# Performance work log

Hardware: AMD Instinct MI355X
Metric: run time of the kernel (lower is better)

Reference implementation:

```python
import jax, jax.numpy as jnp
import numpy as np

N_NODES = 50000


def setup_inputs() -> dict:
    key = jax.random.key(0)
    ks = jax.random.split(key, 6)
    E = 640000
    H = 128
    data = jax.random.normal(ks[0], (N_NODES, H), dtype=jnp.float32)
    edge = jax.random.randint(ks[1], (2, E), 0, N_NODES, dtype=jnp.int64)
    att = jax.random.uniform(ks[2], (E,), dtype=jnp.float32)
    w1 = jax.random.normal(ks[3], (2 * H, H), dtype=jnp.float32) * (1.0 / np.sqrt(2 * H))
    b1 = jnp.zeros((H,), dtype=jnp.float32)
    w2 = jax.random.normal(ks[4], (2 * H, H), dtype=jnp.float32) * (1.0 / np.sqrt(2 * H))
    b2 = jnp.zeros((H,), dtype=jnp.float32)
    return {"data": data, "edge": edge, "att": att, "w1": w1, "b1": b1, "w2": w2, "b2": b2}


def _simple_conv_mean_cat(x, edge, att):
    # PyG SimpleConv(aggr='mean', combine_root='cat') with scalar edge weights.
    src, dst = edge[0], edge[1]
    msgs = x[src] * att[:, None]                               # [E, H] gather + scale
    summed = jax.ops.segment_sum(msgs, dst, num_segments=N_NODES)   # [N, H]
    deg = jax.ops.segment_sum(jnp.ones_like(att), dst, num_segments=N_NODES)  # [N]
    agg = summed / jnp.maximum(deg, 1.0)[:, None]              # mean over incoming edges
    return jnp.concatenate([x, agg], axis=-1)                  # [N, 2H]


def reference(data, edge, att, w1, b1, w2, b2):
    out = _simple_conv_mean_cat(data, edge, att)
    out = jax.nn.relu(out @ w1 + b1)
    out = _simple_conv_mean_cat(out, edge, att)
    out = jax.nn.relu(out @ w2 + b2)
    return out
```

## Files before the change

### kernel.cpp

```cpp
#include <hip/hip_runtime.h>


#define HDIM 128
#define CAP 32
#define FCH 2048

typedef __bf16 bf16x8 __attribute__((ext_vector_type(8)));
typedef float floatx4 __attribute__((ext_vector_type(4)));

__device__ __forceinline__ unsigned short f2bf(float f) {
    unsigned int u = __float_as_uint(f);
    unsigned int r = (u + 0x7fff + ((u >> 16) & 1)) >> 16;
    return (unsigned short)r;
}
__device__ __forceinline__ float bf2f(unsigned short b) {
    return __uint_as_float((unsigned int)b << 16);
}

__global__ __launch_bounds__(256) void k_setup(int* __restrict__ cursor, int nz,
                                               const float* __restrict__ data,
                                               unsigned short* __restrict__ data_bf, int n4,
                                               const float* __restrict__ w1,
                                               unsigned short* __restrict__ w1t,
                                               const float* __restrict__ w2,
                                               unsigned short* __restrict__ w2t,
                                               int zb, int cb) {
    int b = blockIdx.x;
    int t = threadIdx.x;
    if (b < zb) {
        int i = b * 256 + t;
        if (i < nz) cursor[i] = 0;
        return;
    }
    b -= zb;
    if (b < cb) {
        int i = b * 256 + t;
        if (i < n4) {
            float4 v = ((const float4*)data)[i];
            ushort4 o;
            o.x = f2bf(v.x); o.y = f2bf(v.y); o.z = f2bf(v.z); o.w = f2bf(v.w);
            ((ushort4*)data_bf)[i] = o;
        }
        return;
    }
    b -= cb;
    {
        const float* w = (b < 128) ? w1 : w2;
        unsigned short* wt = (b < 128) ? w1t : w2t;
        int bb = (b < 128) ? b : b - 128;
        int idx = bb * 256 + t;
        int k = idx >> 7;
        int n = idx & 127;
        wt[(size_t)n * 256 + k] = f2bf(w[(size_t)k * 128 + n]);
    }
}

__global__ __launch_bounds__(256) void k_fill(const int* __restrict__ edge, int E,
                                              const float* __restrict__ att,
                                              int* __restrict__ cursor,
                                              int* __restrict__ ovf_cnt,
                                              unsigned int* __restrict__ pse,
                                              float4* __restrict__ ovf, int rsize) {
    __shared__ int s_or;
    int t = threadIdx.x;
    if (t == 0) s_or = 0;
    __syncthreads();
    int nw = 2 * E < 512 ? 2 * E : 512;
    int iw = t * 2 + 1;
    int vw = (iw < nw) ? edge[iw] : 0;
    if (vw != 0) atomicOr(&s_or, 1);
    __syncthreads();
    int sh = (s_or == 0) ? 1 : 0;

    int r = blockIdx.x & 7;
    int c = blockIdx.x >> 3;
    int lo = r * rsize;
    int hi = lo + rsize;
    int e0 = c * FCH;
    int e1 = min(E, e0 + FCH);

    for (int e = e0 + t; e < e1; e += 256) {
        int d = edge[(size_t)(E + e) << sh];
        if (d >= lo && d < hi) {
            int s = edge[(size_t)e << sh];
            float a = att[e];
            int slot = atomicAdd(&cursor[d], 1);
            if (slot < CAP) {
                unsigned int rec = ((unsigned int)f2bf(a) << 16) | (unsigned int)(s & 0xffff);
                pse[(size_t)d * CAP + slot] = rec;
            } else {
                int oi = atomicAdd(ovf_cnt, 1);
                ovf[oi] = make_float4(__int_as_float(d), __int_as_float(s), a, 0.f);
            }
        }
    }
}

__global__ __launch_bounds__(128) void k_agg(const unsigned short* __restrict__ x,
                                             const unsigned int* __restrict__ pse,
                                             const int* __restrict__ cursor,
                                             const int* __restrict__ ovf_cnt,
                                             const float4* __restrict__ ovf,
                                             unsigned short* __restrict__ agg, int N) {
    int wave = threadIdx.x >> 6;
    int lane = threadIdx.x & 63;
    int half = lane >> 5;
    int l32 = lane & 31;
    int n = blockIdx.x * 2 + wave;
    bool valid = n < N;
    int deg = valid ? cursor[n] : 0;
    int m = min(deg, CAP);

    __shared__ unsigned int sp[2][CAP];
    if (lane < m) sp[wave][lane] = pse[(size_t)n * CAP + lane];
    __syncthreads();

    const unsigned short* xb = x + 4 * l32;
    float s0 = 0.f, s1 = 0.f, s2 = 0.f, s3 = 0.f;

#define ACC(u, a)                                                   \
    do {                                                            \
        s0 = fmaf(bf2f((unsigned short)((u).x & 0xffff)), (a), s0); \
        s1 = fmaf(bf2f((unsigned short)((u).x >> 16)), (a), s1);    \
        s2 = fmaf(bf2f((unsigned short)((u).y & 0xffff)), (a), s2); \
        s3 = fmaf(bf2f((unsigned short)((u).y >> 16)), (a), s3);    \
    } while (0)
#define ROWP(rec) (xb + (size_t)((rec) & 0xffff) * HDIM)
#define ATT(rec) bf2f((unsigned short)((rec) >> 16))

    int j = 0;
    for (; j + 8 <= m; j += 8) {
        unsigned int rA = sp[wave][j + 0 + half];
        unsigned int rB = sp[wave][j + 2 + half];
        unsigned int rC = sp[wave][j + 4 + half];
        unsigned int rD = sp[wave][j + 6 + half];
        uint2 uA = *(const uint2*)ROWP(rA);
        uint2 uB = *(const uint2*)ROWP(rB);
        uint2 uC = *(const uint2*)ROWP(rC);
        uint2 uD = *(const uint2*)ROWP(rD);
        ACC(uA, ATT(rA));
        ACC(uB, ATT(rB));
        ACC(uC, ATT(rC));
        ACC(uD, ATT(rD));
    }
    for (; j + 2 <= m; j += 2) {
        unsigned int rr = sp[wave][j + half];
        uint2 u = *(const uint2*)ROWP(rr);
        ACC(u, ATT(rr));
    }
    if (j < m && half == 0) {
        unsigned int rr = sp[wave][j];
        uint2 u = *(const uint2*)ROWP(rr);
        ACC(u, ATT(rr));
    }

    int oc = ovf_cnt[0];
    if (oc > 0 && valid) {
        for (int k = half; k < oc; k += 2) {
            float4 f = ovf[k];
            if (__float_as_int(f.x) == n) {
                uint2 u = *(const uint2*)(xb + (size_t)__float_as_int(f.y) * HDIM);
                ACC(u, f.z);
            }
        }
    }
#undef ACC
#undef ROWP
#undef ATT

    s0 += __shfl_xor(s0, 32);
    s1 += __shfl_xor(s1, 32);
    s2 += __shfl_xor(s2, 32);
    s3 += __shfl_xor(s3, 32);

    if (valid && half == 0) {
        float md = fmaxf((float)deg, 1.0f);
        ushort4 o;
        o.x = f2bf(s0 / md);
        o.y = f2bf(s1 / md);
        o.z = f2bf(s2 / md);
        o.w = f2bf(s3 / md);
        *(ushort4*)(agg + (size_t)n * HDIM + 4 * l32) = o;
    }
}

__global__ __launch_bounds__(256) void k_gemm_mfma(const unsigned short* __restrict__ X,
                                                   const unsigned short* __restrict__ AGG,
                                                   const unsigned short* __restrict__ Wt,
                                                   const float* __restrict__ bias,
                                                   float* __restrict__ outF,
                                                   unsigned short* __restrict__ outB,
                                                   int M) {
    __shared__ __align__(16) unsigned short sW[128 * 256];

    int tid = threadIdx.x;
    int wave = tid >> 6;
    int lane = tid & 63;
    int l16 = lane & 15;
    int quad = lane >> 4;

#pragma unroll
    for (int it = 0; it < 16; ++it) {
        int chunk = it * 256 + tid;
        int row = chunk >> 5;
        int c5 = chunk & 31;
        int kc = c5 >> 2;
        int q = c5 & 3;
        int qs = q ^ (row & 3);
        uint4 v = *(const uint4*)(Wt + (size_t)chunk * 8);
        *(uint4*)(sW + row * 256 + kc * 32 + qs * 8) = v;
    }

    int row = blockIdx.x * 64 + wave * 16 + l16;
    int rowA = min(row, M - 1);
    const unsigned short* xrow = X + (size_t)rowA * HDIM + quad * 8;
    const unsigned short* arow = AGG + (size_t)rowA * HDIM + quad * 8;
    bf16x8 af[8];
#pragma unroll
    for (int kc = 0; kc < 4; ++kc) af[kc] = *(const bf16x8*)(xrow + kc * 32);
#pragma unroll
    for (int kc = 4; kc < 8; ++kc) af[kc] = *(const bf16x8*)(arow + (kc - 4) * 32);

    __syncthreads();

    floatx4 acc[8];
#pragma unroll
    for (int c = 0; c < 8; ++c) acc[c] = (floatx4){0.f, 0.f, 0.f, 0.f};

#pragma unroll
    for (int kc = 0; kc < 8; ++kc) {
#pragma unroll
        for (int c = 0; c < 8; ++c) {
            int rb = c * 16 + l16;
            int qs = quad ^ (rb & 3);
            bf16x8 bfr = *(const bf16x8*)(sW + rb * 256 + kc * 32 + qs * 8);
            acc[c] = __builtin_amdgcn_mfma_f32_16x16x32_bf16(af[kc], bfr, acc[c], 0, 0, 0);
        }
    }

    int orow0 = blockIdx.x * 64 + wave * 16 + quad * 4;
#pragma unroll
    for (int c = 0; c < 8; ++c) {
        int col = c * 16 + l16;
        float bv = bias[col];
#pragma unroll
        for (int r = 0; r < 4; ++r) {
            int orow = orow0 + r;
            if (orow < M) {
                float v = fmaxf(acc[c][r] + bv, 0.f);
                if (outF) outF[(size_t)orow * 128 + col] = v;
                else outB[(size_t)orow * 128 + col] = f2bf(v);
            }
        }
    }
}

extern "C" void kernel_launch(void* const* d_in, const int* in_sizes, int n_in,
                              void* d_out, int out_size, void* d_ws, size_t ws_size,
                              hipStream_t stream) {
    const float* data = (const float*)d_in[0];
    const int* edge = (const int*)d_in[1];
    const float* att = (const float*)d_in[2];
    const float* w1 = (const float*)d_in[3];
    const float* b1 = (const float*)d_in[4];
    const float* w2 = (const float*)d_in[5];
    const float* b2 = (const float*)d_in[6];

    const int N = in_sizes[0] / HDIM;
    const int E = in_sizes[1] / 2;

    char* ws = (char*)d_ws;
    size_t o = 0;
    auto carve = [&](size_t bytes) -> char* {
        char* r = ws + o;
        o = (o + bytes + 255) & ~(size_t)255;
        return r;
    };
    int* cursor = (int*)carve((size_t)(N + 4) * 4);
    int* ovf_cnt = cursor + N;
    unsigned int* pse = (unsigned int*)carve((size_t)N * CAP * 4);
    float4* ovf = (float4*)carve((size_t)E * 16);
    unsigned short* data_bf = (unsigned short*)carve((size_t)N * 128 * 2);
    unsigned short* w1t = (unsigned short*)carve(256 * 128 * 2);
    unsigned short* w2t = (unsigned short*)carve(256 * 128 * 2);
    unsigned short* agg_bf = (unsigned short*)carve((size_t)N * 128 * 2);
    unsigned short* out1_bf = (unsigned short*)carve((size_t)N * 128 * 2);
    float* outF = (float*)d_out;

    int nz = N + 4;
    int zb = (nz + 255) / 256;
    int n4 = N * 128 / 4;
    int cb = (n4 + 255) / 256;
    k_setup<<<zb + cb + 256, 256, 0, stream>>>(cursor, nz, data, data_bf, n4,
                                               w1, w1t, w2, w2t, zb, cb);

    int rsize = (N + 7) / 8;
    int nch = (E + FCH - 1) / FCH;
    k_fill<<<nch * 8, 256, 0, stream>>>(edge, E, att, cursor, ovf_cnt, pse, ovf, rsize);

    int ga = (N + 1) / 2;
    int gb = (N + 63) / 64;
    k_agg<<<ga, 128, 0, stream>>>(data_bf, pse, cursor, ovf_cnt, ovf, agg_bf, N);
    k_gemm_mfma<<<gb, 256, 0, stream>>>(data_bf, agg_bf, w1t, b1, nullptr, out1_bf, N);
    k_agg<<<ga, 128, 0, stream>>>(out1_bf, pse, cursor, ovf_cnt, ovf, agg_bf, N);
    k_gemm_mfma<<<gb, 256, 0, stream>>>(out1_bf, agg_bf, w2t, b2, outF, nullptr, N);
}
```

Measured before the change: 214.9 us.

## Widen agg gathers to 16-byte loads and fuse bf16 conversion into fill kernel

New measurement: 212.4 us. No clear change (-1.2%).

```diff
diff --git a/kernel.cpp b/kernel.cpp
--- a/kernel.cpp
+++ b/kernel.cpp
@@ -17,22 +17,62 @@
     return __uint_as_float((unsigned int)b << 16);
 }
 
-__global__ __launch_bounds__(256) void k_setup(int* __restrict__ cursor, int nz,
-                                               const float* __restrict__ data,
-                                               unsigned short* __restrict__ data_bf, int n4,
-                                               const float* __restrict__ w1,
-                                               unsigned short* __restrict__ w1t,
-                                               const float* __restrict__ w2,
-                                               unsigned short* __restrict__ w2t,
-                                               int zb, int cb) {
+__global__ __launch_bounds__(256) void k_zero(int* __restrict__ p, int n) {
+    int i = blockIdx.x * 256 + threadIdx.x;
+    if (i < n) p[i] = 0;
+}
+
+__global__ __launch_bounds__(256) void k_fill(const int* __restrict__ edge, int E,
+                                              const float* __restrict__ att,
+                                              int* __restrict__ cursor,
+                                              int* __restrict__ ovf_cnt,
+                                              unsigned int* __restrict__ pse,
+                                              float4* __restrict__ ovf, int rsize,
+                                              int nfb,
+                                              const float* __restrict__ data,
+                                              unsigned short* __restrict__ data_bf, int n4,
+                                              int cb,
+                                              const float* __restrict__ w1,
+                                              unsigned short* __restrict__ w1t,
+                                              const float* __restrict__ w2,
+                                              unsigned short* __restrict__ w2t) {
     int b = blockIdx.x;
     int t = threadIdx.x;
-    if (b < zb) {
-        int i = b * 256 + t;
-        if (i < nz) cursor[i] = 0;
+    if (b < nfb) {
+        __shared__ int s_or;
+        if (t == 0) s_or = 0;
+        __syncthreads();
+        int nw = 2 * E < 512 ? 2 * E : 512;
+        int iw = t * 2 + 1;
+        int vw = (iw < nw) ? edge[iw] : 0;
+        if (vw != 0) atomicOr(&s_or, 1);
+        __syncthreads();
+        int sh = (s_or == 0) ? 1 : 0;
+
+        int r = b & 7;
+        int c = b >> 3;
+        int lo = r * rsize;
+        int hi = lo + rsize;
+        int e0 = c * FCH;
+        int e1 = min(E, e0 + FCH);
+        for (int e = e0 + t; e < e1; e += 256) {
+            int d = edge[(size_t)(E + e) << sh];
+            if (d >= lo && d < hi) {
+                int s = edge[(size_t)e << sh];
+                float a = att[e];
+                int slot = atomicAdd(&cursor[d], 1);
+                if (slot < CAP) {
+                    unsigned int rec = ((unsigned int)f2bf(a) << 16) | (unsigned int)(s & 0xffff);
+                    pse[(size_t)d * CAP + slot] = rec;
+                } else {
+                    int oi = atomicAdd(ovf_cnt, 1);
+                    ovf[oi] = make_float4(__int_as_float(d), __int_as_float(s), a, 0.f);
+                }
+            }
+        }
         return;
     }
-    b -= zb;
+    b -= nfb;
     if (b < cb) {
         int i = b * 256 + t;
         if (i < n4) {
@@ -55,47 +95,6 @@
     }
 }
 
-__global__ __launch_bounds__(256) void k_fill(const int* __restrict__ edge, int E,
-                                              const float* __restrict__ att,
-                                              int* __restrict__ cursor,
-                                              int* __restrict__ ovf_cnt,
-                                              unsigned int* __restrict__ pse,
-                                              float4* __restrict__ ovf, int rsize) {
-    __shared__ int s_or;
-    int t = threadIdx.x;
-    if (t == 0) s_or = 0;
-    __syncthreads();
-    int nw = 2 * E < 512 ? 2 * E : 512;
-    int iw = t * 2 + 1;
-    int vw = (iw < nw) ? edge[iw] : 0;
-    if (vw != 0) atomicOr(&s_or, 1);
-    __syncthreads();
-    int sh = (s_or == 0) ? 1 : 0;
-
-    int r = blockIdx.x & 7;
-    int c = blockIdx.x >> 3;
-    int lo = r * rsize;
-    int hi = lo + rsize;
-    int e0 = c * FCH;
-    int e1 = min(E, e0 + FCH);
-
-    for (int e = e0 + t; e < e1; e += 256) {
-        int d = edge[(size_t)(E + e) << sh];
-        if (d >= lo && d < hi) {
-            int s = edge[(size_t)e << sh];
-            float a = att[e];
-            int slot = atomicAdd(&cursor[d], 1);
-            if (slot < CAP) {
-                unsigned int rec = ((unsigned int)f2bf(a) << 16) | (unsigned int)(s & 0xffff);
-                pse[(size_t)d * CAP + slot] = rec;
-            } else {
-                int oi = atomicAdd(ovf_cnt, 1);
-                ovf[oi] = make_float4(__int_as_float(d), __int_as_float(s), a, 0.f);
-            }
-        }
-    }
-}
-
 __global__ __launch_bounds__(128) void k_agg(const unsigned short* __restrict__ x,
                                              const unsigned int* __restrict__ pse,
                                              const int* __restrict__ cursor,
@@ -104,8 +103,8 @@
                                              unsigned short* __restrict__ agg, int N) {
     int wave = threadIdx.x >> 6;
     int lane = threadIdx.x & 63;
-    int half = lane >> 5;
-    int l32 = lane & 31;
+    int qw = lane >> 4;
+    int l16 = lane & 15;
     int n = blockIdx.x * 2 + wave;
     bool valid = n < N;
     int deg = valid ? cursor[n] : 0;
@@ -115,72 +114,69 @@
     if (lane < m) sp[wave][lane] = pse[(size_t)n * CAP + lane];
     __syncthreads();
 
-    const unsigned short* xb = x + 4 * l32;
-    float s0 = 0.f, s1 = 0.f, s2 = 0.f, s3 = 0.f;
-
-#define ACC(u, a)                                                   \
+    const unsigned short* xb = x + 8 * l16;
+    float s0 = 0.f, s1 = 0.f, s2 = 0.f, s3 = 0.f, s4 = 0.f, s5 = 0.f, s6 = 0.f, s7 = 0.f;
+
+#define ACC8(u, a)                                                  \
     do {                                                            \
         s0 = fmaf(bf2f((unsigned short)((u).x & 0xffff)), (a), s0); \
         s1 = fmaf(bf2f((unsigned short)((u).x >> 16)), (a), s1);    \
         s2 = fmaf(bf2f((unsigned short)((u).y & 0xffff)), (a), s2); \
         s3 = fmaf(bf2f((unsigned short)((u).y >> 16)), (a), s3);    \
+        s4 = fmaf(bf2f((unsigned short)((u).z & 0xffff)), (a), s4); \
+        s5 = fmaf(bf2f((unsigned short)((u).z >> 16)), (a), s5);    \
+        s6 = fmaf(bf2f((unsigned short)((u).w & 0xffff)), (a), s6); \
+        s7 = fmaf(bf2f((unsigned short)((u).w >> 16)), (a), s7);    \
     } while (0)
-#define ROWP(rec) (xb + (size_t)((rec) & 0xffff) * HDIM)
-#define ATT(rec) bf2f((unsigned short)((rec) >> 16))
-
-    int j = 0;
-    for (; j + 8 <= m; j += 8) {
-        unsigned int rA = sp[wave][j + 0 + half];
-        unsigned int rB = sp[wave][j + 2 + half];
-        unsigned int rC = sp[wave][j + 4 + half];
-        unsigned int rD = sp[wave][j + 6 + half];
-        uint2 uA = *(const uint2*)ROWP(rA);
-        uint2 uB = *(const uint2*)ROWP(rB);
-        uint2 uC = *(const uint2*)ROWP(rC);
-        uint2 uD = *(const uint2*)ROWP(rD);
-        ACC(uA, ATT(rA));
-        ACC(uB, ATT(rB));
-        ACC(uC, ATT(rC));
-        ACC(uD, ATT(rD));
-    }
-    for (; j + 2 <= m; j += 2) {
-        unsigned int rr = sp[wave][j + half];
-        uint2 u = *(const uint2*)ROWP(rr);
-        ACC(u, ATT(rr));
-    }
-    if (j < m && half == 0) {
-        unsigned int rr = sp[wave][j];
-        uint2 u = *(const uint2*)ROWP(rr);
-        ACC(u, ATT(rr));
+
+    for (int j = 0; j < m; j += 16) {
+        int i0 = j + qw;
+        int i1 = j + 4 + qw;
+        int i2 = j + 8 + qw;
+        int i3 = j + 12 + qw;
+        unsigned int r0 = (i0 < m) ? sp[wave][i0] : 0u;
+        unsigned int r1 = (i1 < m) ? sp[wave][i1] : 0u;
+        unsigned int r2 = (i2 < m) ? sp[wave][i2] : 0u;
+        unsigned int r3 = (i3 < m) ? sp[wave][i3] : 0u;
+        uint4 u0 = *(const uint4*)(xb + (size_t)(r0 & 0xffff) * HDIM);
+        uint4 u1 = *(const uint4*)(xb + (size_t)(r1 & 0xffff) * HDIM);
+        uint4 u2 = *(const uint4*)(xb + (size_t)(r2 & 0xffff) * HDIM);
+        uint4 u3 = *(const uint4*)(xb + (size_t)(r3 & 0xffff) * HDIM);
+        ACC8(u0, bf2f((unsigned short)(r0 >> 16)));
+        ACC8(u1, bf2f((unsigned short)(r1 >> 16)));
+        ACC8(u2, bf2f((unsigned short)(r2 >> 16)));
+        ACC8(u3, bf2f((unsigned short)(r3 >> 16)));
     }
 
     int oc = ovf_cnt[0];
     if (oc > 0 && valid) {
-        for (int k = half; k < oc; k += 2) {
+        for (int k = qw; k < oc; k += 4) {
             float4 f = ovf[k];
             if (__float_as_int(f.x) == n) {
-                uint2 u = *(const uint2*)(xb + (size_t)__float_as_int(f.y) * HDIM);
-                ACC(u, f.z);
+                uint4 u = *(const uint4*)(xb + (size_t)__float_as_int(f.y) * HDIM);
+                ACC8(u, f.z);
             }
         }
     }
-#undef ACC
-#undef ROWP
-#undef ATT
-
-    s0 += __shfl_xor(s0, 32);
-    s1 += __shfl_xor(s1, 32);
-    s2 += __shfl_xor(s2, 32);
-    s3 += __shfl_xor(s3, 32);
-
-    if (valid && half == 0) {
+#undef ACC8
+
+    s0 += __shfl_xor(s0, 16); s0 += __shfl_xor(s0, 32);
+    s1 += __shfl_xor(s1, 16); s1 += __shfl_xor(s1, 32);
+    s2 += __shfl_xor(s2, 16); s2 += __shfl_xor(s2, 32);
+    s3 += __shfl_xor(s3, 16); s3 += __shfl_xor(s3, 32);
+    s4 += __shfl_xor(s4, 16); s4 += __shfl_xor(s4, 32);
+    s5 += __shfl_xor(s5, 16); s5 += __shfl_xor(s5, 32);
+    s6 += __shfl_xor(s6, 16); s6 += __shfl_xor(s6, 32);
+    s7 += __shfl_xor(s7, 16); s7 += __shfl_xor(s7, 32);
+
+    if (valid && qw == 0) {
         float md = fmaxf((float)deg, 1.0f);
-        ushort4 o;
-        o.x = f2bf(s0 / md);
-        o.y = f2bf(s1 / md);
-        o.z = f2bf(s2 / md);
-        o.w = f2bf(s3 / md);
-        *(ushort4*)(agg + (size_t)n * HDIM + 4 * l32) = o;
+        uint4 o;
+        o.x = (unsigned int)f2bf(s0 / md) | ((unsigned int)f2bf(s1 / md) << 16);
+        o.y = (unsigned int)f2bf(s2 / md) | ((unsigned int)f2bf(s3 / md) << 16);
+        o.z = (unsigned int)f2bf(s4 / md) | ((unsigned int)f2bf(s5 / md) << 16);
+        o.w = (unsigned int)f2bf(s6 / md) | ((unsigned int)f2bf(s7 / md) << 16);
+        *(uint4*)(agg + (size_t)n * HDIM + 8 * l16) = o;
     }
 }
 
@@ -288,15 +284,16 @@
     float* outF = (float*)d_out;
 
     int nz = N + 4;
-    int zb = (nz + 255) / 256;
+    k_zero<<<(nz + 255) / 256, 256, 0, stream>>>(cursor, nz);
+
+    int rsize = (N + 7) / 8;
+    int nch = (E + FCH - 1) / FCH;
+    int nfb = nch * 8;
     int n4 = N * 128 / 4;
     int cb = (n4 + 255) / 256;
-    k_setup<<<zb + cb + 256, 256, 0, stream>>>(cursor, nz, data, data_bf, n4,
-                                               w1, w1t, w2, w2t, zb, cb);
-
-    int rsize = (N + 7) / 8;
-    int nch = (E + FCH - 1) / FCH;
-    k_fill<<<nch * 8, 256, 0, stream>>>(edge, E, att, cursor, ovf_cnt, pse, ovf, rsize);
+    k_fill<<<nfb + cb + 256, 256, 0, stream>>>(edge, E, att, cursor, ovf_cnt, pse, ovf,
+                                               rsize, nfb, data, data_bf, n4, cb,
+                                               w1, w1t, w2, w2t);
 
     int ga = (N + 1) / 2;
     int gb = (N + 63) / 64;
```
